# Kernel optimization log

Hardware: AMD Instinct MI355X
Metric: run time of the kernel (lower is better)

The kernel has to match this reference:

```python
import jax, jax.numpy as jnp
import numpy as np

B, N, D = 8, 2048, 192
G, S = 512, 32
OUT = 384
ALPHA, BETA = 1000.0, 100.0
EPS = 1e-05


def setup_inputs() -> dict:
    key = jax.random.key(0)
    ks = jax.random.split(key, 8)
    sc = 0.02
    return {
        "points": jax.random.normal(ks[0], (B, N, 3), jnp.float32),
        "feats": jax.random.normal(ks[1], (B, N, D), jnp.float32),
        # 1x1 conv weights (BN assumed folded, inference form)
        "W1": sc * jax.random.normal(ks[2], (OUT, 2 * D), jnp.float32),
        "b1": jnp.zeros((OUT,), jnp.float32),
        "Wa": sc * jax.random.normal(ks[3], (OUT // 2, OUT), jnp.float32),
        "ba": jnp.zeros((OUT // 2,), jnp.float32),
        "Wb": sc * jax.random.normal(ks[4], (OUT, OUT // 2), jnp.float32),
        "bb": jnp.zeros((OUT,), jnp.float32),
    }


def fps(pts, n_samples):
    """Farthest point sampling. pts: (B,N,3) -> idx (B,n_samples) int32."""
    def one(p):  # (N,3)
        def step(carry, _):
            dists, last = carry
            cur = p[last]                                 # (3,)
            d = jnp.sum((p - cur) ** 2, axis=-1)          # (N,)
            dists = jnp.minimum(dists, d)
            nxt = jnp.argmax(dists).astype(jnp.int32)
            return (dists, nxt), last
        init = (jnp.full((p.shape[0],), jnp.inf, p.dtype), jnp.int32(0))
        _, idxs = jax.lax.scan(step, init, None, length=n_samples)
        return idxs
    return jax.vmap(one)(pts)


def pairwise_sqdist(a, b):
    # a: (B,G,3), b: (B,N,3) -> (B,G,N)
    aa = jnp.sum(a * a, -1)[:, :, None]
    bb = jnp.sum(b * b, -1)[:, None, :]
    return aa + bb - 2.0 * jnp.einsum('bgd,bnd->bgn', a, b)


def group_points(x, idx):
    # x: (B,N,C), idx: (B,G,S) -> (B,G,S,C)
    return jax.vmap(lambda f, i: f[i])(x, idx)


def pos_embed(xyz):
    # xyz: (B,G,S,3) -> (B,G,S,OUT)  Fourier positional encoding
    in_dim = xyz.shape[-1]
    feat_dim = OUT // (2 * in_dim)
    freq = jnp.arange(feat_dim, dtype=xyz.dtype)
    denom = jnp.power(jnp.asarray(ALPHA, xyz.dtype), freq / feat_dim)
    z = BETA * xyz[..., None] / denom                      # (B,G,S,3,feat_dim)
    pos = jnp.concatenate([jnp.sin(z), jnp.cos(z)], axis=-1)
    return pos.reshape(*xyz.shape[:-1], OUT)


def _forward(points, feats, W1, b1, Wa, ba, Wb, bb):
    # FPS centers
    fps_idx = fps(points, G)                               # (B,G)
    centers = jax.vmap(lambda p, i: p[i])(points, fps_idx)  # (B,G,3)

    d2 = pairwise_sqdist(centers, points)                  # (B,G,N)
    _, knn_idx = jax.lax.top_k(-d2, S)                     # (B,G,S)

    neighbor_pts = group_points(points, knn_idx)           # (B,G,S,3)
    neighbor_feats = group_points(feats, knn_idx)          # (B,G,S,D)

    # 'sim' normalization: global (scalar, unbiased) std of centered neighbors
    diff = neighbor_pts - centers[:, :, None, :]
    m = jnp.mean(diff)
    std = jnp.sqrt(jnp.sum((diff - m) ** 2) / (diff.size - 1))
    neighbor_pts = diff / (std + EPS)

    # center feats via 1-NN of centers in points
    center_idx = jnp.argmin(d2, axis=-1)                   # (B,G)
    center_feats = jax.vmap(lambda f, i: f[i])(feats, center_idx)  # (B,G,D)

    # concat neighbor + broadcast center feats -> (B,G,S,2D)
    gf = jnp.concatenate(
        [neighbor_feats, jnp.broadcast_to(center_feats[:, :, None, :], (points.shape[0], G, S, D))],
        axis=-1)

    # shared MLP (1x1 conv) + ReLU
    gf = jax.nn.relu(jnp.einsum('bgsc,oc->bgso', gf, W1) + b1)  # (B,G,S,OUT)

    pos = pos_embed(neighbor_pts)                          # (B,G,S,OUT)
    gf = (gf + pos) * pos

    # residual block: conv(OUT->OUT/2)+ReLU, conv(OUT/2->OUT), +x, ReLU
    h = jax.nn.relu(jnp.einsum('bgso,ho->bgsh', gf, Wa) + ba)
    h = jnp.einsum('bgsh,oh->bgso', h, Wb) + bb
    gf = jax.nn.relu(h + gf)

    # fused max + mean pooling over neighbors (S)
    out = jnp.max(gf, axis=2) + jnp.mean(gf, axis=2)       # (B,G,OUT)
    return centers, out


def reference(points, feats, W1, b1, Wa, ba, Wb, bb):
    return _forward(points, feats, W1, b1, Wa, ba, Wb, bb)
```

## Files before the change

### kernel.cpp

```cpp
#include <hip/hip_runtime.h>
#include <math.h>

#define Bn   8
#define Nn   2048
#define Dn   192
#define Gn   512
#define Sn   32
#define OUTn 384
#define Mrows (Bn * Gn * Sn)

typedef __attribute__((ext_vector_type(8))) unsigned short ushortx8;
typedef __attribute__((ext_vector_type(8))) __bf16 bf16x8;
typedef __attribute__((ext_vector_type(4))) float floatx4;

static constexpr size_t OFF_KNN   = 0;
static constexpr size_t OFF_CIDX  = 524288;
static constexpr size_t OFF_DIFF  = 540672;
static constexpr size_t OFF_SUMS  = 2113536;
static constexpr size_t OFF_STD   = 2113552;
static constexpr size_t OFF_DENOM = 2113792;
static constexpr size_t OFF_W1B   = 2114048;
static constexpr size_t OFF_WAB   = 2408960;
static constexpr size_t OFF_WBB   = 2556416;
static constexpr size_t OFF_G1    = 2703872;
static constexpr size_t OFF_FEATB = 103367168;

__device__ __forceinline__ unsigned short f2bf(float f) {
  unsigned u = __float_as_uint(f);
  unsigned r = (u + 0x7FFFu + ((u >> 16) & 1u)) >> 16;
  return (unsigned short)r;
}
__device__ __forceinline__ float bf2f(unsigned short h) {
  return __uint_as_float(((unsigned)h) << 16);
}
__device__ __forceinline__ floatx4 mfma_bf16(ushortx8 a, ushortx8 b, floatx4 c) {
  return __builtin_amdgcn_mfma_f32_16x16x32_bf16(
      __builtin_bit_cast(bf16x8, a), __builtin_bit_cast(bf16x8, b), c, 0, 0, 0);
}

__device__ __forceinline__ void gld16(const void* g, void* l) {
  __builtin_amdgcn_global_load_lds(
      (const __attribute__((address_space(1))) unsigned int*)g,
      (__attribute__((address_space(3))) unsigned int*)l, 16, 0, 0);
}

template <int CTRL>
__device__ __forceinline__ float dpp_max(float v) {
  int o = __builtin_amdgcn_update_dpp(0, __float_as_int(v), CTRL, 0xf, 0xf, true);
  return fmaxf(v, __int_as_float(o));
}

__global__ void prep_kernel(const float* __restrict__ W1, const float* __restrict__ Wa,
                            const float* __restrict__ Wb, const float* __restrict__ feats,
                            unsigned short* __restrict__ W1b, unsigned short* __restrict__ Wab,
                            unsigned short* __restrict__ Wbb, unsigned short* __restrict__ featb,
                            float* __restrict__ rdenomTab) {
  int i = blockIdx.x * 256 + threadIdx.x;
  if (i < 147456)            W1b[i] = f2bf(W1[i]);
  else if (i < 221184)       Wab[i - 147456] = f2bf(Wa[i - 147456]);
  else if (i < 294912)       Wbb[i - 221184] = f2bf(Wb[i - 221184]);
  else if (i < 3440640)      featb[i - 294912] = f2bf(feats[i - 294912]);
  if (blockIdx.x == 0 && threadIdx.x < 64)
    rdenomTab[threadIdx.x] = (float)(1.0 / pow(1000.0, (double)threadIdx.x / 64.0));
}

__global__ __launch_bounds__(256) void fps_kernel(const float* __restrict__ points,
                                                  float* __restrict__ centers) {
  const int b = blockIdx.x;
  const int t = threadIdx.x;
  const int w = t >> 6, lane = t & 63;
  __shared__ float4 p4[Nn];
  __shared__ unsigned long long wkey[2][4];

  const float* P = points + (size_t)b * Nn * 3;
  for (int n = t; n < Nn; n += 256) {
    float x = P[n * 3], y = P[n * 3 + 1], z = P[n * 3 + 2];
    p4[n] = make_float4(x, y, z, 0.f);
  }
  __syncthreads();

  float rx[8], ry[8], rz[8], dist[8];
#pragma unroll
  for (int k = 0; k < 8; ++k) {
    float4 p = p4[t * 8 + k];
    rx[k] = p.x; ry[k] = p.y; rz[k] = p.z;
    dist[k] = INFINITY;
  }

  int cur = 0;
  for (int it = 0; it < Gn; ++it) {
    const float4 c = p4[cur];
    if (t == 0) {
      float* cd = centers + ((size_t)b * Gn + it) * 3;
      cd[0] = c.x; cd[1] = c.y; cd[2] = c.z;
    }
    float bv = -1.0f;
#pragma unroll
    for (int k = 0; k < 8; ++k) {
      float dx = __fsub_rn(rx[k], c.x);
      float dy = __fsub_rn(ry[k], c.y);
      float dz = __fsub_rn(rz[k], c.z);
      float d = __fadd_rn(__fadd_rn(__fmul_rn(dx, dx), __fmul_rn(dy, dy)), __fmul_rn(dz, dz));
      dist[k] = fminf(dist[k], d);
      bv = fmaxf(bv, dist[k]);
    }
    int li = 7;
#pragma unroll
    for (int k = 6; k >= 0; --k) li = (dist[k] == bv) ? k : li;

    float red = bv;
    red = dpp_max<0x111>(red);
    red = dpp_max<0x112>(red);
    red = dpp_max<0x114>(red);
    red = dpp_max<0x118>(red);
    red = dpp_max<0x142>(red);
    red = dpp_max<0x143>(red);
    const float M = __int_as_float(__builtin_amdgcn_readlane(__float_as_int(red), 63));

    unsigned long long msk = __ballot(bv == M);
    const int L = __ffsll((long long)msk) - 1;
    const int liL = __builtin_amdgcn_readlane(li, L);
    const int idx = (w * 64 + L) * 8 + liL;

    unsigned long long key =
        ((unsigned long long)__float_as_uint(M) << 32) | (unsigned)(0x7FFFFFFF - idx);
    if (lane == 0) wkey[it & 1][w] = key;
    __syncthreads();
    unsigned long long k0 = wkey[it & 1][0];
    unsigned long long k1 = wkey[it & 1][1];
    unsigned long long k2 = wkey[it & 1][2];
    unsigned long long k3 = wkey[it & 1][3];
    unsigned long long m01 = (k1 > k0) ? k1 : k0;
    unsigned long long m23 = (k3 > k2) ? k3 : k2;
    unsigned long long mm = (m23 > m01) ? m23 : m01;
    cur = 0x7FFFFFFF - (int)(unsigned)mm;
  }
}

__global__ __launch_bounds__(256) void knn_kernel(const float* __restrict__ points,
                                                  const float* __restrict__ centers,
                                                  int* __restrict__ knn, int* __restrict__ cidx,
                                                  float* __restrict__ diffb,
                                                  double* __restrict__ sums) {
  const int t = threadIdx.x;
  const int w = t >> 6, lane = t & 63;
  const int bg = blockIdx.x * 4 + w;
  const int b = bg >> 9;

  const float* P = points + (size_t)b * Nn * 3;
  const float* cc = centers + (size_t)bg * 3;
  const float cx = cc[0], cy = cc[1], cz = cc[2];
  const float aa = __fadd_rn(__fadd_rn(__fmul_rn(cx, cx), __fmul_rn(cy, cy)), __fmul_rn(cz, cz));

  unsigned key[32];
#pragma unroll 8
  for (int s = 0; s < 32; ++s) {
    const int n = s * 64 + lane;
    float X = P[n * 3], Y = P[n * 3 + 1], Z = P[n * 3 + 2];
    float bbv = __fadd_rn(__fadd_rn(__fmul_rn(X, X), __fmul_rn(Y, Y)), __fmul_rn(Z, Z));
    float dot = __fadd_rn(__fadd_rn(__fmul_rn(cx, X), __fmul_rn(cy, Y)), __fmul_rn(cz, Z));
    float d2 = __fsub_rn(__fadd_rn(aa, bbv), __fmul_rn(2.0f, dot));
    unsigned u = __float_as_uint(d2);
    key[s] = u ^ ((unsigned)((int)u >> 31) | 0x80000000u);
  }

  unsigned mk = key[0]; int ms = 0;
#pragma unroll
  for (int s = 1; s < 32; ++s)
    if (key[s] < mk) { mk = key[s]; ms = s; }

  int mysel = 0;
  for (int it = 0; it < Sn; ++it) {
    unsigned long long p = ((unsigned long long)mk << 32) | (unsigned)(ms * 64 + lane);
#pragma unroll
    for (int off = 1; off <= 32; off <<= 1) {
      unsigned long long o = __shfl_xor(p, off, 64);
      p = (o < p) ? o : p;
    }
    const int n_win = (int)(unsigned)p;
    if (lane == it) mysel = n_win;
    if (lane == (n_win & 63)) {
      const int sw = n_win >> 6;
#pragma unroll
      for (int s = 0; s < 32; ++s)
        if (s == sw) key[s] = 0xFFFFFFFFu;
      mk = key[0]; ms = 0;
#pragma unroll
      for (int s = 1; s < 32; ++s)
        if (key[s] < mk) { mk = key[s]; ms = s; }
    }
  }

  double s1 = 0.0, s2 = 0.0;
  if (lane < Sn) {
    knn[(size_t)bg * Sn + lane] = mysel;
    float X = P[mysel * 3], Y = P[mysel * 3 + 1], Z = P[mysel * 3 + 2];
    float dx = __fsub_rn(X, cx), dy = __fsub_rn(Y, cy), dz = __fsub_rn(Z, cz);
    float* db = diffb + (size_t)bg * 96 + lane * 3;
    db[0] = dx; db[1] = dy; db[2] = dz;
    s1 = (double)dx + (double)dy + (double)dz;
    s2 = (double)dx * (double)dx + (double)dy * (double)dy + (double)dz * (double)dz;
  }
#pragma unroll
  for (int off = 1; off <= 32; off <<= 1) {
    s1 += __shfl_xor(s1, off, 64);
    s2 += __shfl_xor(s2, off, 64);
  }
  if (lane == 0) {
    cidx[bg] = __shfl(mysel, 0, 64);
    atomicAdd(sums, s1);
    atomicAdd(sums + 1, s2);
  }
}

__global__ void stddev_kernel(const double* __restrict__ sums, float* __restrict__ stdp) {
  const double n = (double)(Bn * Gn * Sn * 3);
  double s1 = sums[0], s2 = sums[1];
  double mean = s1 / n;
  double var = (s2 - s1 * mean) / (n - 1.0);
  float stdf = (float)sqrt(var) + 1e-5f;
  *stdp = (float)(1.0 / (double)stdf);
}

__global__ __launch_bounds__(256) void gemm1_kernel(
    const unsigned short* __restrict__ featb, const unsigned short* __restrict__ W1b,
    const float* __restrict__ b1, const int* __restrict__ knn,
    const int* __restrict__ cidx, const float* __restrict__ diffb,
    const float* __restrict__ rstd_p, const float* __restrict__ rdenomTab,
    unsigned short* __restrict__ G1) {
  __shared__ unsigned short As[128 * 64];
  __shared__ unsigned short Bs[128 * 64];
  const int t = threadIdx.x;
  const int bm = blockIdx.x, bn = blockIdx.y;
  const int wid = t >> 6, lane = t & 63, quad = lane >> 4, c16 = lane & 15;
  const int wr = wid >> 1, wc = wid & 1;

  int aOffN[4], aOffC[4], bOff[4];
#pragma unroll
  for (int i = 0; i < 4; ++i) {
    const int slot = i * 256 + t;
    const int row = slot >> 3, segV = slot & 7;
    const int seg = segV ^ (row & 7);
    const int grow = bm * 128 + row;
    const int bg = grow >> 5, s = grow & 31, bb_ = bg >> 9;
    const int nidx = knn[(size_t)bg * Sn + s];
    const int ci = cidx[bg];
    aOffN[i] = (bb_ * Nn + nidx) * Dn + seg * 8;
    aOffC[i] = (bb_ * Nn + ci) * Dn + seg * 8;
    bOff[i] = (bn * 128 + row) * 384 + seg * 8;
  }

  floatx4 acc[4][4];
#pragma unroll
  for (int i = 0; i < 4; ++i)
#pragma unroll
    for (int j = 0; j < 4; ++j) acc[i][j] = (floatx4){0.f, 0.f, 0.f, 0.f};

  for (int kt = 0; kt < 6; ++kt) {
    const int kb = kt * 64;
#pragma unroll
    for (int i = 0; i < 4; ++i) {
      const unsigned short* srcA =
          (kt < 3) ? (featb + aOffN[i] + kb) : (featb + aOffC[i] + (kb - 192));
      gld16(srcA, &As[(i * 256 + wid * 64) * 8]);
      gld16(W1b + bOff[i] + kb, &Bs[(i * 256 + wid * 64) * 8]);
    }
    __syncthreads();
#pragma unroll
    for (int ks = 0; ks < 2; ++ks) {
      ushortx8 af[4], bf[4];
#pragma unroll
      for (int mt = 0; mt < 4; ++mt) {
        const int row = wr * 64 + mt * 16 + c16;
        const int seg = (ks * 4 + quad) ^ (row & 7);
        af[mt] = *(const ushortx8*)&As[row * 64 + seg * 8];
      }
#pragma unroll
      for (int nt = 0; nt < 4; ++nt) {
        const int row = wc * 64 + nt * 16 + c16;
        const int seg = (ks * 4 + quad) ^ (row & 7);
        bf[nt] = *(const ushortx8*)&Bs[row * 64 + seg * 8];
      }
#pragma unroll
      for (int mt = 0; mt < 4; ++mt)
#pragma unroll
        for (int nt = 0; nt < 4; ++nt)
          acc[mt][nt] = mfma_bf16(af[mt], bf[nt], acc[mt][nt]);
    }
    __syncthreads();
  }

  const float rstd = *rstd_p;
  float bias[4], rdnm[4];
  bool usin[4];
#pragma unroll
  for (int nt = 0; nt < 4; ++nt) {
    const int col = bn * 128 + wc * 64 + nt * 16 + c16;
    bias[nt] = b1[col];
    const int j = col & 127;
    usin[nt] = (j < 64);
    rdnm[nt] = rdenomTab[j & 63];
  }
#pragma unroll
  for (int mt = 0; mt < 4; ++mt) {
#pragma unroll
    for (int r = 0; r < 4; ++r) {
      const int row = bm * 128 + wr * 64 + mt * 16 + quad * 4 + r;
      const float dv = diffb[(size_t)row * 3 + bn];
      const float x = __fmul_rn(dv, rstd);
      const float zb = __fmul_rn(100.0f, x);
#pragma unroll
      for (int nt = 0; nt < 4; ++nt) {
        const int col = bn * 128 + wc * 64 + nt * 16 + c16;
        float y = fmaxf(acc[mt][nt][r] + bias[nt], 0.f);
        float z = __fmul_rn(zb, rdnm[nt]);
        float p = usin[nt] ? __sinf(z) : __cosf(z);
        float g = (y + p) * p;
        G1[(size_t)row * 384 + col] = f2bf(g);
      }
    }
  }
}

__global__ __launch_bounds__(512) void gemm23_kernel(
    const unsigned short* __restrict__ G1, const unsigned short* __restrict__ Wab,
    const float* __restrict__ ba, const unsigned short* __restrict__ Wbb,
    const float* __restrict__ bb, float* __restrict__ outp) {
  __shared__ __align__(16) char smem[100352];
  unsigned short* Htile = (unsigned short*)smem;
  unsigned short* As    = (unsigned short*)(smem + 51200);
  unsigned short* BsA   = (unsigned short*)(smem + 51200 + 16384);
  unsigned short* BsB   = (unsigned short*)(smem + 51200);

  const int t = threadIdx.x;
  const int bm = blockIdx.x;
  const int lane = t & 63, quad = lane >> 4, c16 = lane & 15;
  const int wid = t >> 6;
  const int wr = wid >> 2, wc = wid & 3;

  int aOff[2], bOffA[3];
#pragma unroll
  for (int i = 0; i < 2; ++i) {
    const int slot = i * 512 + t;
    const int row = slot >> 3, segV = slot & 7;
    aOff[i] = (bm * 128 + row) * 384 + (segV ^ (row & 7)) * 8;
  }
#pragma unroll
  for (int i = 0; i < 3; ++i) {
    const int slot = i * 512 + t;
    const int row = slot >> 3, segV = slot & 7;
    bOffA[i] = row * 384 + (segV ^ (row & 7)) * 8;
  }

  floatx4 accA[4][3];
#pragma unroll
  for (int i = 0; i < 4; ++i)
#pragma unroll
    for (int j = 0; j < 3; ++j) accA[i][j] = (floatx4){0.f, 0.f, 0.f, 0.f};

  for (int kt = 0; kt < 6; ++kt) {
    const int kb = kt * 64;
#pragma unroll
    for (int i = 0; i < 2; ++i) gld16(G1 + aOff[i] + kb, As + ((size_t)(i * 512 + t)) * 8);
#pragma unroll
    for (int i = 0; i < 3; ++i) gld16(Wab + bOffA[i] + kb, BsA + ((size_t)(i * 512 + t)) * 8);
    __syncthreads();
#pragma unroll
    for (int ks = 0; ks < 2; ++ks) {
      ushortx8 af[4], bf[3];
#pragma unroll
      for (int mt = 0; mt < 4; ++mt) {
        const int row = wr * 64 + mt * 16 + c16;
        const int seg = (ks * 4 + quad) ^ (row & 7);
        af[mt] = *(const ushortx8*)&As[row * 64 + seg * 8];
      }
#pragma unroll
      for (int nt = 0; nt < 3; ++nt) {
        const int row = wc * 48 + nt * 16 + c16;
        const int seg = (ks * 4 + quad) ^ (row & 7);
        bf[nt] = *(const ushortx8*)&BsA[row * 64 + seg * 8];
      }
#pragma unroll
      for (int mt = 0; mt < 4; ++mt)
#pragma unroll
        for (int nt = 0; nt < 3; ++nt)
          accA[mt][nt] = mfma_bf16(af[mt], bf[nt], accA[mt][nt]);
    }
    __syncthreads();
  }

#pragma unroll
  for (int nt = 0; nt < 3; ++nt) {
    const int col = wc * 48 + nt * 16 + c16;
    const float bias = ba[col];
#pragma unroll
    for (int mt = 0; mt < 4; ++mt)
#pragma unroll
      for (int r = 0; r < 4; ++r) {
        const int row = wr * 64 + mt * 16 + quad * 4 + r;
        Htile[row * 200 + col] = f2bf(fmaxf(accA[mt][nt][r] + bias, 0.f));
      }
  }
  __syncthreads();

  int bOffB[6];
#pragma unroll
  for (int i = 0; i < 6; ++i) {
    const int slot = i * 512 + t;
    const int row = slot >> 3, segV = slot & 7;
    bOffB[i] = row * 192 + (segV ^ (row & 7)) * 8;
  }

  floatx4 acc[4][6];
#pragma unroll
  for (int i = 0; i < 4; ++i)
#pragma unroll
    for (int j = 0; j < 6; ++j) acc[i][j] = (floatx4){0.f, 0.f, 0.f, 0.f};

  for (int kt = 0; kt < 3; ++kt) {
    const int kb = kt * 64;
#pragma unroll
    for (int i = 0; i < 6; ++i) gld16(Wbb + bOffB[i] + kb, BsB + ((size_t)(i * 512 + t)) * 8);
    __syncthreads();
#pragma unroll
    for (int ks = 0; ks < 2; ++ks) {
      ushortx8 af[4], bf[6];
#pragma unroll
      for (int mt = 0; mt < 4; ++mt) {
        const int row = wr * 64 + mt * 16 + c16;
        af[mt] = *(const ushortx8*)&Htile[row * 200 + kb + ks * 32 + quad * 8];
      }
#pragma unroll
      for (int nt = 0; nt < 6; ++nt) {
        const int row = wc * 96 + nt * 16 + c16;
        const int seg = (ks * 4 + quad) ^ (row & 7);
        bf[nt] = *(const ushortx8*)&BsB[row * 64 + seg * 8];
      }
#pragma unroll
      for (int mt = 0; mt < 4; ++mt)
#pragma unroll
        for (int nt = 0; nt < 6; ++nt)
          acc[mt][nt] = mfma_bf16(af[mt], bf[nt], acc[mt][nt]);
    }
    __syncthreads();
  }

#pragma unroll
  for (int nt = 0; nt < 6; ++nt) {
    const int col = wc * 96 + nt * 16 + c16;
    const float bias = bb[col];
    float gmax[2] = {-INFINITY, -INFINITY};
    float gsum[2] = {0.f, 0.f};
#pragma unroll
    for (int mt = 0; mt < 4; ++mt) {
      const int grp = mt >> 1;
#pragma unroll
      for (int r = 0; r < 4; ++r) {
        const int row = bm * 128 + wr * 64 + mt * 16 + quad * 4 + r;
        float v = acc[mt][nt][r] + bias + bf2f(G1[(size_t)row * 384 + col]);
        v = fmaxf(v, 0.f);
        gmax[grp] = fmaxf(gmax[grp], v);
        gsum[grp] += v;
      }
    }
#pragma unroll
    for (int grp = 0; grp < 2; ++grp) {
      float m = gmax[grp], su = gsum[grp];
#pragma unroll
      for (int off = 16; off <= 32; off <<= 1) {
        m = fmaxf(m, __shfl_xor(m, off, 64));
        su += __shfl_xor(su, off, 64);
      }
      if (quad == 0) {
        const int bg = bm * 4 + wr * 2 + grp;
        outp[(size_t)bg * 384 + col] = m + su / 32.0f;
      }
    }
  }
}

extern "C" void kernel_launch(void* const* d_in, const int* in_sizes, int n_in,
                              void* d_out, int out_size, void* d_ws, size_t ws_size,
                              hipStream_t stream) {
  const float* points = (const float*)d_in[0];
  const float* feats  = (const float*)d_in[1];
  const float* W1 = (const float*)d_in[2];
  const float* b1 = (const float*)d_in[3];
  const float* Wa = (const float*)d_in[4];
  const float* ba = (const float*)d_in[5];
  const float* Wb = (const float*)d_in[6];
  const float* bb = (const float*)d_in[7];
  float* outF = (float*)d_out;

  char* ws = (char*)d_ws;
  int*            knn      = (int*)(ws + OFF_KNN);
  int*            cidx     = (int*)(ws + OFF_CIDX);
  float*          diffb    = (float*)(ws + OFF_DIFF);
  double*         sums     = (double*)(ws + OFF_SUMS);
  float*          stdp     = (float*)(ws + OFF_STD);
  float*          rdenomTab= (float*)(ws + OFF_DENOM);
  unsigned short* W1b      = (unsigned short*)(ws + OFF_W1B);
  unsigned short* Wab      = (unsigned short*)(ws + OFF_WAB);
  unsigned short* Wbb      = (unsigned short*)(ws + OFF_WBB);
  unsigned short* G1       = (unsigned short*)(ws + OFF_G1);
  unsigned short* featb    = (unsigned short*)(ws + OFF_FEATB);

  hipMemsetAsync(sums, 0, 2 * sizeof(double), stream);
  prep_kernel<<<13440, 256, 0, stream>>>(W1, Wa, Wb, feats, W1b, Wab, Wbb, featb, rdenomTab);
  fps_kernel<<<Bn, 256, 0, stream>>>(points, outF);
  knn_kernel<<<Bn * Gn / 4, 256, 0, stream>>>(points, outF, knn, cidx, diffb, sums);
  stddev_kernel<<<1, 1, 0, stream>>>(sums, stdp);
  gemm1_kernel<<<dim3(Mrows / 128, 3), 256, 0, stream>>>(featb, W1b, b1, knn, cidx,
                                                         diffb, stdp, rdenomTab, G1);
  gemm23_kernel<<<Mrows / 128, 512, 0, stream>>>(G1, Wab, ba, Wbb, bb, outF + Bn * Gn * 3);
}
```

Measured before the change: 556.6 us.

## Fuse prep into FPS kernel, widen FPS to 512 threads, fold stddev into knn

Merges the bf16 weight/feature conversion into the same launch as farthest point sampling, so the 8 FPS blocks run alongside the conversion blocks instead of serially after them. FPS now uses 512 threads with 4 points per thread, which shortens per-iteration work but needs an 8-way cross-wave reduction. The separate stddev kernel is removed: the last knn block, found through an atomic counter, computes the inverse std. This trades one fewer launch and better overlap for the threadfence/atomic overhead and the wider per-iteration sync.

```diff
diff --git a/kernel.cpp b/kernel.cpp
--- a/kernel.cpp
+++ b/kernel.cpp
@@ -18,6 +18,7 @@
 static constexpr size_t OFF_DIFF  = 540672;
 static constexpr size_t OFF_SUMS  = 2113536;
 static constexpr size_t OFF_STD   = 2113552;
+static constexpr size_t OFF_CNT   = 2113568;
 static constexpr size_t OFF_DENOM = 2113792;
 static constexpr size_t OFF_W1B   = 2114048;
 static constexpr size_t OFF_WAB   = 2408960;
@@ -50,39 +51,46 @@
   return fmaxf(v, __int_as_float(o));
 }
 
-__global__ void prep_kernel(const float* __restrict__ W1, const float* __restrict__ Wa,
-                            const float* __restrict__ Wb, const float* __restrict__ feats,
-                            unsigned short* __restrict__ W1b, unsigned short* __restrict__ Wab,
-                            unsigned short* __restrict__ Wbb, unsigned short* __restrict__ featb,
-                            float* __restrict__ rdenomTab) {
-  int i = blockIdx.x * 256 + threadIdx.x;
-  if (i < 147456)            W1b[i] = f2bf(W1[i]);
-  else if (i < 221184)       Wab[i - 147456] = f2bf(Wa[i - 147456]);
-  else if (i < 294912)       Wbb[i - 221184] = f2bf(Wb[i - 221184]);
-  else if (i < 3440640)      featb[i - 294912] = f2bf(feats[i - 294912]);
-  if (blockIdx.x == 0 && threadIdx.x < 64)
-    rdenomTab[threadIdx.x] = (float)(1.0 / pow(1000.0, (double)threadIdx.x / 64.0));
-}
-
-__global__ __launch_bounds__(256) void fps_kernel(const float* __restrict__ points,
-                                                  float* __restrict__ centers) {
+__global__ __launch_bounds__(512) void fps_prep_kernel(
+    const float* __restrict__ points, float* __restrict__ centers,
+    const float* __restrict__ W1, const float* __restrict__ Wa,
+    const float* __restrict__ Wb, const float* __restrict__ feats,
+    unsigned short* __restrict__ W1b, unsigned short* __restrict__ Wab,
+    unsigned short* __restrict__ Wbb, unsigned short* __restrict__ featb,
+    float* __restrict__ rdenomTab) {
+  const int t = threadIdx.x;
+
+  if (blockIdx.x >= 8) {
+    const int base = (blockIdx.x - 8) * 2048 + t;
+#pragma unroll
+    for (int j = 0; j < 4; ++j) {
+      const int i = base + j * 512;
+      if (i < 147456)        W1b[i] = f2bf(W1[i]);
+      else if (i < 221184)   Wab[i - 147456] = f2bf(Wa[i - 147456]);
+      else if (i < 294912)   Wbb[i - 221184] = f2bf(Wb[i - 221184]);
+      else                   featb[i - 294912] = f2bf(feats[i - 294912]);
+    }
+    if (blockIdx.x == 8 && t < 64)
+      rdenomTab[t] = (float)(1.0 / pow(1000.0, (double)t / 64.0));
+    return;
+  }
+
   const int b = blockIdx.x;
-  const int t = threadIdx.x;
   const int w = t >> 6, lane = t & 63;
   __shared__ float4 p4[Nn];
-  __shared__ unsigned long long wkey[2][4];
+  __shared__ unsigned long long wkey[2][8];
 
   const float* P = points + (size_t)b * Nn * 3;
-  for (int n = t; n < Nn; n += 256) {
+  for (int n = t; n < Nn; n += 512) {
     float x = P[n * 3], y = P[n * 3 + 1], z = P[n * 3 + 2];
     p4[n] = make_float4(x, y, z, 0.f);
   }
   __syncthreads();
 
-  float rx[8], ry[8], rz[8], dist[8];
-#pragma unroll
-  for (int k = 0; k < 8; ++k) {
-    float4 p = p4[t * 8 + k];
+  float rx[4], ry[4], rz[4], dist[4];
+#pragma unroll
+  for (int k = 0; k < 4; ++k) {
+    float4 p = p4[t * 4 + k];
     rx[k] = p.x; ry[k] = p.y; rz[k] = p.z;
     dist[k] = INFINITY;
   }
@@ -96,7 +104,7 @@
     }
     float bv = -1.0f;
 #pragma unroll
-    for (int k = 0; k < 8; ++k) {
+    for (int k = 0; k < 4; ++k) {
       float dx = __fsub_rn(rx[k], c.x);
       float dy = __fsub_rn(ry[k], c.y);
       float dz = __fsub_rn(rz[k], c.z);
@@ -104,9 +112,9 @@
       dist[k] = fminf(dist[k], d);
       bv = fmaxf(bv, dist[k]);
     }
-    int li = 7;
-#pragma unroll
-    for (int k = 6; k >= 0; --k) li = (dist[k] == bv) ? k : li;
+    int li = 3;
+#pragma unroll
+    for (int k = 2; k >= 0; --k) li = (dist[k] == bv) ? k : li;
 
     float red = bv;
     red = dpp_max<0x111>(red);
@@ -120,20 +128,22 @@
     unsigned long long msk = __ballot(bv == M);
     const int L = __ffsll((long long)msk) - 1;
     const int liL = __builtin_amdgcn_readlane(li, L);
-    const int idx = (w * 64 + L) * 8 + liL;
+    const int idx = (w * 64 + L) * 4 + liL;
 
     unsigned long long key =
         ((unsigned long long)__float_as_uint(M) << 32) | (unsigned)(0x7FFFFFFF - idx);
-    if (lane == 0) wkey[it & 1][w] = key;
-    __syncthreads();
-    unsigned long long k0 = wkey[it & 1][0];
-    unsigned long long k1 = wkey[it & 1][1];
-    unsigned long long k2 = wkey[it & 1][2];
-    unsigned long long k3 = wkey[it & 1][3];
-    unsigned long long m01 = (k1 > k0) ? k1 : k0;
-    unsigned long long m23 = (k3 > k2) ? k3 : k2;
-    unsigned long long mm = (m23 > m01) ? m23 : m01;
-    cur = 0x7FFFFFFF - (int)(unsigned)mm;
+    const int buf = it & 1;
+    if (lane == 0) wkey[buf][w] = key;
+    __syncthreads();
+    unsigned long long kk[8];
+#pragma unroll
+    for (int i = 0; i < 8; ++i) kk[i] = wkey[buf][i];
+#pragma unroll
+    for (int stride = 1; stride < 8; stride <<= 1)
+#pragma unroll
+      for (int i = 0; i < 8; i += 2 * stride)
+        kk[i] = (kk[i + stride] > kk[i]) ? kk[i + stride] : kk[i];
+    cur = 0x7FFFFFFF - (int)(unsigned)kk[0];
   }
 }
 
@@ -141,7 +151,9 @@
                                                   const float* __restrict__ centers,
                                                   int* __restrict__ knn, int* __restrict__ cidx,
                                                   float* __restrict__ diffb,
-                                                  double* __restrict__ sums) {
+                                                  double* __restrict__ sums,
+                                                  int* __restrict__ cnt,
+                                                  float* __restrict__ stdp) {
   const int t = threadIdx.x;
   const int w = t >> 6, lane = t & 63;
   const int bg = blockIdx.x * 4 + w;
@@ -211,15 +223,21 @@
     atomicAdd(sums, s1);
     atomicAdd(sums + 1, s2);
   }
-}
-
-__global__ void stddev_kernel(const double* __restrict__ sums, float* __restrict__ stdp) {
-  const double n = (double)(Bn * Gn * Sn * 3);
-  double s1 = sums[0], s2 = sums[1];
-  double mean = s1 / n;
-  double var = (s2 - s1 * mean) / (n - 1.0);
-  float stdf = (float)sqrt(var) + 1e-5f;
-  *stdp = (float)(1.0 / (double)stdf);
+  __threadfence();
+  __syncthreads();
+  if (t == 0) {
+    const int old = atomicAdd(cnt, 1);
+    if (old == (Bn * Gn / 4) - 1) {
+      __threadfence();
+      const double S1 = atomicAdd(sums, 0.0);
+      const double S2 = atomicAdd(sums + 1, 0.0);
+      const double n = (double)(Bn * Gn * Sn * 3);
+      const double mean = S1 / n;
+      const double var = (S2 - S1 * mean) / (n - 1.0);
+      const float stdf = (float)sqrt(var) + 1e-5f;
+      *stdp = (float)(1.0 / (double)stdf);
+    }
+  }
 }
 
 __global__ __launch_bounds__(256) void gemm1_kernel(
@@ -498,6 +516,7 @@
   float*          diffb    = (float*)(ws + OFF_DIFF);
   double*         sums     = (double*)(ws + OFF_SUMS);
   float*          stdp     = (float*)(ws + OFF_STD);
+  int*            cnt      = (int*)(ws + OFF_CNT);
   float*          rdenomTab= (float*)(ws + OFF_DENOM);
   unsigned short* W1b      = (unsigned short*)(ws + OFF_W1B);
   unsigned short* Wab      = (unsigned short*)(ws + OFF_WAB);
@@ -505,11 +524,11 @@
   unsigned short* G1       = (unsigned short*)(ws + OFF_G1);
   unsigned short* featb    = (unsigned short*)(ws + OFF_FEATB);
 
-  hipMemsetAsync(sums, 0, 2 * sizeof(double), stream);
-  prep_kernel<<<13440, 256, 0, stream>>>(W1, Wa, Wb, feats, W1b, Wab, Wbb, featb, rdenomTab);
-  fps_kernel<<<Bn, 256, 0, stream>>>(points, outF);
-  knn_kernel<<<Bn * Gn / 4, 256, 0, stream>>>(points, outF, knn, cidx, diffb, sums);
-  stddev_kernel<<<1, 1, 0, stream>>>(sums, stdp);
+  hipMemsetAsync(ws + OFF_SUMS, 0, 40, stream);
+  fps_prep_kernel<<<8 + 1680, 512, 0, stream>>>(points, outF, W1, Wa, Wb, feats,
+                                                W1b, Wab, Wbb, featb, rdenomTab);
+  knn_kernel<<<Bn * Gn / 4, 256, 0, stream>>>(points, outF, knn, cidx, diffb,
+                                              sums, cnt, stdp);
   gemm1_kernel<<<dim3(Mrows / 128, 3), 256, 0, stream>>>(featb, W1b, b1, knn, cidx,
                                                          diffb, stdp, rdenomTab, G1);
   gemm23_kernel<<<Mrows / 128, 512, 0, stream>>>(G1, Wab, ba, Wbb, bb, outF + Bn * Gn * 3);
```

Measured after the change: 675.5 us. 1.21x slower.
